# Performance work log

Hardware: AMD Instinct MI355X
Metric: run time of the kernel (lower is better)

## Reference

```python
import jax, jax.numpy as jnp
import numpy as np

B, H, L, D = 16, 8, 512, 64
TEMPERATURE = 8.0  # sqrt(d_k)
MASK_SENTINEL = -10000.0
BIG_NEG = 1e9


def setup_inputs() -> dict:
    key = jax.random.key(0)
    kq, kk, kv, km = jax.random.split(key, 4)
    q = jax.random.normal(kq, (B * H, L, D), dtype=jnp.float32)
    k = jax.random.normal(kk, (B * H, L, D), dtype=jnp.float32)
    v = jax.random.normal(kv, (B * H, L, D), dtype=jnp.float32)
    mask = jnp.where(jax.random.bernoulli(km, 0.1, (B, L)), MASK_SENTINEL, 0.0).astype(jnp.float32)
    return {"q": q, "k": k, "v": v, "mask": mask, "n_head": H}


def reference(q, k, v, mask, n_head):
    # attn: [B*H, L, L]
    attn = jnp.einsum("bid,bjd->bij", q, k) / TEMPERATURE
    # masked_fill(mask == -10000, 1e9); other values subtracted as-is
    m = jnp.where(mask == MASK_SENTINEL, BIG_NEG, mask)          # [B, L]
    m_bh = jnp.repeat(m, n_head, axis=0)                          # [B*H, L], matches reshape(B*H, ...)
    # row mask (mask.unsqueeze(-1).repeat) and its transpose (column mask)
    attn = attn - m_bh[:, :, None] - m_bh[:, None, :]
    attn = jax.nn.softmax(attn, axis=2)
    # dropout in eval mode (identity) for the deterministic reference
    output = jnp.einsum("bij,bjd->bid", attn, v)
    return output, attn
```

## Files before the change

### kernel.cpp

```cpp
#include <hip/hip_runtime.h>
#include <stdint.h>

#define Ln 512
#define Dn 64
#define BHn 128
#define AOFF ((size_t)BHn*Ln*Dn)

typedef __attribute__((ext_vector_type(8))) short short8;
typedef __attribute__((ext_vector_type(4))) float f32x4;
typedef __attribute__((ext_vector_type(4))) unsigned int u32x4;
typedef __attribute__((ext_vector_type(2))) unsigned int u32x2;

__device__ __forceinline__ uint16_t f2bf(float f){
  uint32_t x = __float_as_uint(f);
  return (uint16_t)((x + 0x7FFFu + ((x>>16)&1u)) >> 16);
}
__device__ __forceinline__ float bf2f(uint16_t u){ return __uint_as_float(((uint32_t)u)<<16); }
__device__ __forceinline__ uint32_t pack2(float a, float b){
  return (uint32_t)f2bf(a) | ((uint32_t)f2bf(b)<<16);
}
__device__ __forceinline__ void gld16(const uint16_t* g, uint16_t* l){
  __builtin_amdgcn_global_load_lds(
      (const __attribute__((address_space(1))) void*)g,
      (__attribute__((address_space(3))) void*)l, 16, 0, 0);
}

extern "C" __global__ __launch_bounds__(256)
void attn_prep(const float* __restrict__ kg, const float* __restrict__ vg,
               uint16_t* __restrict__ khw, uint16_t* __restrict__ klw,
               uint16_t* __restrict__ vtw)
{
  const int t  = threadIdx.x;
  const int cx = blockIdx.x;
  const int c  = cx >> 1;
  const int h  = cx & 1;
  const int bh = blockIdx.y;
  const size_t base = (size_t)bh*(Ln*Dn);
  const size_t wsb  = ((size_t)bh<<15) + ((size_t)c<<13);

  {
    const int sj  = h*64 + (t>>2);
    const int skh = (t>>1)&1;
    const int w2b = (t&1)*2;
    const float* kr = kg + base + (size_t)(c*128 + sj)*Dn + skh*32 + w2b*8;
    const int sx = (sj&7)<<3;
    #pragma unroll
    for (int w=0; w<2; ++w){
      const int w2 = w2b + w;
      f32x4 x0 = *(const f32x4*)(kr + w*8);
      f32x4 x1 = *(const f32x4*)(kr + w*8 + 4);
      uint32_t hw[4], lw[4];
      #pragma unroll
      for (int pi=0; pi<4; ++pi){
        float a0 = (pi<2) ? x0[pi*2]   : x1[(pi-2)*2];
        float a1 = (pi<2) ? x0[pi*2+1] : x1[(pi-2)*2+1];
        uint16_t h0 = f2bf(a0), h1 = f2bf(a1);
        hw[pi] = (uint32_t)h0 | ((uint32_t)h1<<16);
        lw[pi] = (uint32_t)f2bf(a0 - bf2f(h0)) | ((uint32_t)f2bf(a1 - bf2f(h1))<<16);
      }
      const size_t di = wsb + sj*64 + ((skh*32 + w2*8) ^ sx);
      *(u32x4*)(khw + di) = (u32x4){hw[0],hw[1],hw[2],hw[3]};
      *(u32x4*)(klw + di) = (u32x4){lw[0],lw[1],lw[2],lw[3]};
    }
  }

  {
    const int j0 = h*64 + (t>>4)*4;
    const int d0 = (t&15)*4;
    const float* vr = vg + base + (size_t)(c*128 + j0)*Dn + d0;
    f32x4 r0 = *(const f32x4*)(vr);
    f32x4 r1 = *(const f32x4*)(vr + Dn);
    f32x4 r2 = *(const f32x4*)(vr + 2*Dn);
    f32x4 r3 = *(const f32x4*)(vr + 3*Dn);
    #pragma unroll
    for (int qd=0; qd<4; ++qd){
      const int d = d0 + qd;
      u32x2 w; w.x = pack2(r0[qd], r1[qd]); w.y = pack2(r2[qd], r3[qd]);
      *(u32x2*)(vtw + wsb + d*128 + (j0 ^ ((d&7)<<3))) = w;
    }
  }
}

extern "C" __global__ __launch_bounds__(256, 2)
void attn_main2(const float* __restrict__ qg, const float* __restrict__ mg,
                const uint16_t* __restrict__ khw, const uint16_t* __restrict__ klw,
                const uint16_t* __restrict__ vtw, float* __restrict__ outg)
{
  __shared__ __align__(16) uint16_t BIG[32768];
  __shared__ float CMV[512];

  const int t    = threadIdx.x;
  const int lane = t & 63;
  const int wv   = t >> 6;
  const int li   = lane & 15;
  const int lq   = lane >> 4;
  const int kx   = (li&7)<<3;

  const int lin = blockIdx.x + (blockIdx.y << 3);
  const int xcd = lin & 7;
  const int jj  = lin >> 3;
  const int bh  = (xcd << 4) + (jj >> 3);
  const int b   = bh >> 3;
  const int i0  = (jj & 7)*64 + wv*16;

  const size_t base = (size_t)bh*(Ln*Dn);
  const float* mrow = mg + b*Ln;
  const size_t wsbh = (size_t)bh << 15;

  uint16_t* PW = BIG + 16384 + wv*2176;

  auto issueK = [&](int c, int bsel){
    const size_t so = wsbh + ((size_t)c<<13) + (wv<<11) + (lane<<3);
    uint16_t* dh = BIG + bsel*16384 + (wv<<11);
    #pragma unroll
    for (int i=0;i<4;++i){
      gld16(khw + so + i*512, dh + i*512);
      gld16(klw + so + i*512, dh + 8192 + i*512);
    }
  };
  auto issueV = [&](int c, int bsel){
    const size_t so = wsbh + ((size_t)c<<13) + (wv<<11) + (lane<<3);
    uint16_t* dv = BIG + bsel*8192 + (wv<<11);
    #pragma unroll
    for (int i=0;i<4;++i) gld16(vtw + so + i*512, dv + i*512);
  };

  const float* qrow = qg + base + (size_t)(i0 + li)*Dn;
  f32x4 qx0a = *(const f32x4*)(qrow + lq*8);
  f32x4 qx0b = *(const f32x4*)(qrow + lq*8 + 4);
  f32x4 qx1a = *(const f32x4*)(qrow + 32 + lq*8);
  f32x4 qx1b = *(const f32x4*)(qrow + 32 + lq*8 + 4);
  float m0 = mrow[t], m1 = mrow[t+256];
  float mv = mrow[i0 + li];

  issueK(0, 0);

  CMV[t]     = (m0 < -9000.f) ? 1e9f : m0;
  CMV[t+256] = (m1 < -9000.f) ? 1e9f : m1;
  const float rmv = (mv < -9000.f) ? 1e9f : mv;

  short8 qhi[2], qlo[2];
  #pragma unroll
  for (int kt=0; kt<2; ++kt){
    f32x4 xa = kt ? qx1a : qx0a;
    f32x4 xb = kt ? qx1b : qx0b;
    #pragma unroll
    for (int e=0; e<8; ++e){
      float x = (e<4) ? xa[e] : xb[e-4];
      uint16_t h = f2bf(x);
      qhi[kt][e] = (short)h;
      qlo[kt][e] = (short)f2bf(x - bf2f(h));
    }
  }

  f32x4 acc[32];
  #pragma unroll
  for (int j=0; j<32; ++j) acc[j] = (f32x4)0.f;

  #pragma unroll
  for (int c=0; c<4; ++c){
    if (c<3) issueK(c+1, (c+1)&1);
    if (c<3) asm volatile("s_waitcnt vmcnt(8)" ::: "memory");
    else     asm volatile("s_waitcnt vmcnt(4)" ::: "memory");
    __builtin_amdgcn_sched_barrier(0);
    __builtin_amdgcn_s_barrier();
    __builtin_amdgcn_sched_barrier(0);
    const uint16_t* KHp = BIG + (c&1)*16384;
    const uint16_t* KLp = KHp + 8192;
    __builtin_amdgcn_s_setprio(1);
    #pragma unroll
    for (int jt=0; jt<8; ++jt){
      #pragma unroll
      for (int kt=0; kt<2; ++kt){
        const int idx = (jt*16 + li)*64 + ((kt*32 + lq*8) ^ kx);
        short8 kh = *(const short8*)(KHp + idx);
        short8 kl = *(const short8*)(KLp + idx);
        f32x4 A = acc[c*8+jt];
        A = __builtin_amdgcn_mfma_f32_16x16x32_bf16(kh, qhi[kt], A, 0,0,0);
        A = __builtin_amdgcn_mfma_f32_16x16x32_bf16(kl, qhi[kt], A, 0,0,0);
        A = __builtin_amdgcn_mfma_f32_16x16x32_bf16(kh, qlo[kt], A, 0,0,0);
        acc[c*8+jt] = A;
      }
    }
    __builtin_amdgcn_s_setprio(0);
    __builtin_amdgcn_sched_barrier(0);
    __builtin_amdgcn_s_barrier();
    __builtin_amdgcn_sched_barrier(0);
    if (c==2) issueV(0, 0);
  }

  #pragma unroll
  for (int jt=0; jt<32; ++jt){
    f32x4 cm = *(const f32x4*)(CMV + jt*16 + lq*4);
    #pragma unroll
    for (int r=0; r<4; ++r)
      acc[jt][r] = (acc[jt][r]*0.125f - rmv) - cm[r];
  }

  float mx = -3.4e38f;
  #pragma unroll
  for (int jt=0; jt<32; ++jt)
    #pragma unroll
    for (int r=0; r<4; ++r) mx = fmaxf(mx, acc[jt][r]);
  mx = fmaxf(mx, __shfl_xor(mx, 16));
  mx = fmaxf(mx, __shfl_xor(mx, 32));
  float sum = 0.f;
  #pragma unroll
  for (int jt=0; jt<32; ++jt)
    #pragma unroll
    for (int r=0; r<4; ++r){ float e = __expf(acc[jt][r]-mx); acc[jt][r] = e; sum += e; }
  sum += __shfl_xor(sum, 16);
  sum += __shfl_xor(sum, 32);
  const float inv = 1.0f/sum;
  #pragma unroll
  for (int jt=0; jt<32; ++jt) acc[jt] = acc[jt]*inv;

  f32x4 oacc[4];
  #pragma unroll
  for (int dt=0; dt<4; ++dt) oacc[dt] = (f32x4)0.f;

  float* arow = outg + AOFF + (size_t)bh*Ln*Ln + (size_t)(i0+li)*Ln;

  #pragma unroll
  for (int c=0; c<4; ++c){
    u32x2 pwreg[8];
    #pragma unroll
    for (int jtl=0; jtl<8; ++jtl){
      const f32x4 p = acc[c*8+jtl];
      pwreg[jtl].x = pack2(p[0], p[1]);
      pwreg[jtl].y = pack2(p[2], p[3]);
    }
    if (c==0) asm volatile("s_waitcnt vmcnt(0)" ::: "memory");
    else      asm volatile("s_waitcnt vmcnt(8)" ::: "memory");
    __builtin_amdgcn_sched_barrier(0);
    __builtin_amdgcn_s_barrier();
    __builtin_amdgcn_sched_barrier(0);
    if (c<3) issueV(c+1, (c+1)&1);
    #pragma unroll
    for (int jtl=0; jtl<8; ++jtl)
      *(u32x2*)(PW + li*136 + jtl*16 + lq*4) = pwreg[jtl];
    asm volatile("s_waitcnt lgkmcnt(0)" ::: "memory");
    __builtin_amdgcn_sched_barrier(0);
    const uint16_t* VTp = BIG + (c&1)*8192;
    __builtin_amdgcn_s_setprio(1);
    #pragma unroll
    for (int c32=0; c32<4; ++c32){
      short8 pf = *(const short8*)(PW + li*136 + c32*32 + lq*8);
      #pragma unroll
      for (int dt=0; dt<4; ++dt){
        short8 vb = *(const short8*)(VTp + (dt*16+li)*128 + ((c32*32+lq*8) ^ kx));
        oacc[dt] = __builtin_amdgcn_mfma_f32_16x16x32_bf16(vb, pf, oacc[dt], 0,0,0);
      }
    }
    __builtin_amdgcn_s_setprio(0);
    #pragma unroll
    for (int jtl=0; jtl<8; ++jtl)
      *(f32x4*)(arow + (c*8+jtl)*16 + lq*4) = acc[c*8+jtl];
  }

  #pragma unroll
  for (int dt=0; dt<4; ++dt)
    *(f32x4*)(outg + base + (size_t)(i0+li)*Dn + dt*16 + lq*4) = oacc[dt];
}

#define KSTR  72
#define VTSTR 136
#define FPSTRH 136

extern "C" __global__ __launch_bounds__(256, 2)
void attn_mfma(const float* __restrict__ qg, const float* __restrict__ kg,
               const float* __restrict__ vg, const float* __restrict__ mg,
               float* __restrict__ outg)
{
  __shared__ uint4 ldsraw[(36864 + 2048)/16];
  uint16_t* KHI = (uint16_t*)ldsraw;
  uint16_t* KLO = KHI + 128*KSTR;
  uint16_t* VT  = (uint16_t*)ldsraw;
  float*    CMV = (float*)((char*)ldsraw + 36864);

  const int t    = threadIdx.x;
  const int lane = t & 63;
  const int wv   = t >> 6;
  const int li   = lane & 15;
  const int lq   = lane >> 4;

  const int lin = blockIdx.x + (blockIdx.y << 3);
  const int xcd = lin & 7;
  const int jj  = lin >> 3;
  const int bh  = (xcd << 4) + (jj >> 3);
  const int b   = bh >> 3;
  const int i0  = (jj & 7)*64 + wv*16;

  const size_t base = (size_t)bh*(Ln*Dn);
  const float* mrow = mg + b*Ln;

  uint16_t* PW = (uint16_t*)((char*)ldsraw + 17408 + wv*(16*FPSTRH*2));

  {
    float m0 = mrow[t], m1 = mrow[t+256];
    CMV[t]     = (m0 < -9000.f) ? 1e9f : m0;
    CMV[t+256] = (m1 < -9000.f) ? 1e9f : m1;
  }

  short8 qhi[2], qlo[2];
  {
    const float* qrow = qg + base + (size_t)(i0 + li)*Dn;
    #pragma unroll
    for (int kt=0; kt<2; ++kt){
      const float* p = qrow + kt*32 + lq*8;
      f32x4 x0 = *(const f32x4*)p;
      f32x4 x1 = *(const f32x4*)(p+4);
      #pragma unroll
      for (int e=0; e<8; ++e){
        float x = (e<4) ? x0[e] : x1[e-4];
        uint16_t h = f2bf(x);
        qhi[kt][e] = (short)h;
        qlo[kt][e] = (short)f2bf(x - bf2f(h));
      }
    }
  }

  f32x4 acc[32];
  #pragma unroll
  for (int j=0; j<32; ++j) acc[j] = (f32x4)0.f;

  const int sj = t>>1, skh = t&1;
  #pragma unroll
  for (int c=0; c<4; ++c){
    __syncthreads();
    {
      const float* kr = kg + base + (size_t)(c*128 + sj)*Dn + skh*32;
      uint16_t* dhi = KHI + sj*KSTR + skh*32;
      uint16_t* dlo = KLO + sj*KSTR + skh*32;
      #pragma unroll
      for (int w2=0; w2<4; ++w2){
        f32x4 x0 = *(const f32x4*)(kr + w2*8);
        f32x4 x1 = *(const f32x4*)(kr + w2*8 + 4);
        uint32_t hw[4], lw[4];
        #pragma unroll
        for (int pi=0; pi<4; ++pi){
          float a0 = (pi<2) ? x0[pi*2]   : x1[(pi-2)*2];
          float a1 = (pi<2) ? x0[pi*2+1] : x1[(pi-2)*2+1];
          uint16_t h0 = f2bf(a0), h1 = f2bf(a1);
          hw[pi] = (uint32_t)h0 | ((uint32_t)h1<<16);
          lw[pi] = (uint32_t)f2bf(a0 - bf2f(h0)) | ((uint32_t)f2bf(a1 - bf2f(h1))<<16);
        }
        *(u32x4*)(dhi + w2*8) = (u32x4){hw[0],hw[1],hw[2],hw[3]};
        *(u32x4*)(dlo + w2*8) = (u32x4){lw[0],lw[1],lw[2],lw[3]};
      }
    }
    __syncthreads();
    #pragma unroll
    for (int jt=0; jt<8; ++jt){
      #pragma unroll
      for (int kt=0; kt<2; ++kt){
        const int off = (jt*16 + li)*KSTR + kt*32 + lq*8;
        short8 kh = *(const short8*)(KHI + off);
        short8 kl = *(const short8*)(KLO + off);
        f32x4 A = acc[c*8+jt];
        A = __builtin_amdgcn_mfma_f32_16x16x32_bf16(kh, qhi[kt], A, 0,0,0);
        A = __builtin_amdgcn_mfma_f32_16x16x32_bf16(kl, qhi[kt], A, 0,0,0);
        A = __builtin_amdgcn_mfma_f32_16x16x32_bf16(kh, qlo[kt], A, 0,0,0);
        acc[c*8+jt] = A;
      }
    }
  }

  {
    float mv = mrow[i0 + li];
    const float rmv = (mv < -9000.f) ? 1e9f : mv;
    #pragma unroll
    for (int jt=0; jt<32; ++jt){
      f32x4 cm = *(const f32x4*)(CMV + jt*16 + lq*4);
      #pragma unroll
      for (int r=0; r<4; ++r)
        acc[jt][r] = (acc[jt][r]*0.125f - rmv) - cm[r];
    }
  }
  float mx = -3.4e38f;
  #pragma unroll
  for (int jt=0; jt<32; ++jt)
    #pragma unroll
    for (int r=0; r<4; ++r) mx = fmaxf(mx, acc[jt][r]);
  mx = fmaxf(mx, __shfl_xor(mx, 16));
  mx = fmaxf(mx, __shfl_xor(mx, 32));
  float sum = 0.f;
  #pragma unroll
  for (int jt=0; jt<32; ++jt)
    #pragma unroll
    for (int r=0; r<4; ++r){ float e = __expf(acc[jt][r]-mx); acc[jt][r] = e; sum += e; }
  sum += __shfl_xor(sum, 16);
  sum += __shfl_xor(sum, 32);
  const float inv = 1.0f/sum;

  {
    float* arow = outg + AOFF + (size_t)bh*Ln*Ln + (size_t)(i0+li)*Ln;
    #pragma unroll
    for (int jt=0; jt<32; ++jt){
      f32x4 p = acc[jt]*inv;
      acc[jt] = p;
      *(f32x4*)(arow + jt*16 + lq*4) = p;
    }
  }

  f32x4 oacc[4];
  #pragma unroll
  for (int dt=0; dt<4; ++dt) oacc[dt] = (f32x4)0.f;

  #pragma unroll
  for (int c=0; c<4; ++c){
    __syncthreads();
    #pragma unroll
    for (int it=0; it<2; ++it){
      const int j0 = (t>>4)*4 + it*64;
      const int d0 = (t&15)*4;
      const float* vr = vg + base + (size_t)(c*128 + j0)*Dn + d0;
      f32x4 r0 = *(const f32x4*)(vr);
      f32x4 r1 = *(const f32x4*)(vr + Dn);
      f32x4 r2 = *(const f32x4*)(vr + 2*Dn);
      f32x4 r3 = *(const f32x4*)(vr + 3*Dn);
      #pragma unroll
      for (int qd=0; qd<4; ++qd){
        u32x2 w; w.x = pack2(r0[qd], r1[qd]); w.y = pack2(r2[qd], r3[qd]);
        *(u32x2*)(VT + (d0+qd)*VTSTR + j0) = w;
      }
    }
    __syncthreads();
    #pragma unroll
    for (int jtl=0; jtl<8; ++jtl){
      const f32x4 p = acc[c*8+jtl];
      u32x2 w; w.x = pack2(p[0], p[1]); w.y = pack2(p[2], p[3]);
      *(u32x2*)(PW + li*FPSTRH + jtl*16 + lq*4) = w;
    }
    asm volatile("s_waitcnt lgkmcnt(0)" ::: "memory");
    #pragma unroll
    for (int c32=0; c32<4; ++c32){
      short8 pf = *(const short8*)(PW + li*FPSTRH + c32*32 + lq*8);
      #pragma unroll
      for (int dt=0; dt<4; ++dt){
        short8 vb = *(const short8*)(VT + (dt*16+li)*VTSTR + c32*32 + lq*8);
        oacc[dt] = __builtin_amdgcn_mfma_f32_16x16x32_bf16(vb, pf, oacc[dt], 0,0,0);
      }
    }
  }

  #pragma unroll
  for (int dt=0; dt<4; ++dt)
    *(f32x4*)(outg + base + (size_t)(i0+li)*Dn + dt*16 + lq*4) = oacc[dt];
}

extern "C" void kernel_launch(void* const* d_in, const int* in_sizes, int n_in,
                              void* d_out, int out_size, void* d_ws, size_t ws_size,
                              hipStream_t stream)
{
  (void)in_sizes; (void)n_in; (void)out_size;
  const float* qg = (const float*)d_in[0];
  const float* kg = (const float*)d_in[1];
  const float* vg = (const float*)d_in[2];
  const float* mg = (const float*)d_in[3];
  float* outg = (float*)d_out;

  const size_t WS_NEED = 25165824;
  if (d_ws && ws_size >= WS_NEED){
    uint16_t* khw = (uint16_t*)d_ws;
    uint16_t* klw = (uint16_t*)((char*)d_ws + 8388608);
    uint16_t* vtw = (uint16_t*)((char*)d_ws + 16777216);
    attn_prep<<<dim3(8, BHn), 256, 0, stream>>>(kg, vg, khw, klw, vtw);
    attn_main2<<<dim3(Ln/64, BHn), 256, 0, stream>>>(qg, mg, khw, klw, vtw, outg);
  } else {
    attn_mfma<<<dim3(Ln/64, BHn), 256, 0, stream>>>(qg, kg, vg, mg, outg);
  }
}
```

Baseline: 216.2 us.

## Split key dimension across wave pairs with 32-row blocks and triple-buffered K/V

```diff
diff --git a/kernel.cpp b/kernel.cpp
--- a/kernel.cpp
+++ b/kernel.cpp
@@ -30,20 +30,21 @@
                uint16_t* __restrict__ khw, uint16_t* __restrict__ klw,
                uint16_t* __restrict__ vtw)
 {
-  const int t  = threadIdx.x;
-  const int cx = blockIdx.x;
-  const int c  = cx >> 1;
-  const int h  = cx & 1;
-  const int bh = blockIdx.y;
+  const int t   = threadIdx.x;
+  const int lin = blockIdx.x + (blockIdx.y << 3);
+  const int xcd = lin & 7;
+  const int by2 = lin >> 3;
+  const int bh  = (xcd << 4) + (by2 >> 3);
+  const int hc  = by2 & 7;
   const size_t base = (size_t)bh*(Ln*Dn);
-  const size_t wsb  = ((size_t)bh<<15) + ((size_t)c<<13);
-
-  {
-    const int sj  = h*64 + (t>>2);
-    const int skh = (t>>1)&1;
-    const int w2b = (t&1)*2;
-    const float* kr = kg + base + (size_t)(c*128 + sj)*Dn + skh*32 + w2b*8;
-    const int sx = (sj&7)<<3;
+  const size_t wsbh = (size_t)bh << 15;
+
+  {
+    const int grow = hc*64 + (t>>2);
+    const int skh  = (t>>1)&1;
+    const int w2b  = (t&1)*2;
+    const float* kr = kg + base + (size_t)grow*Dn + skh*32 + w2b*8;
+    const int sx = (grow&7)<<3;
     #pragma unroll
     for (int w=0; w<2; ++w){
       const int w2 = w2b + w;
@@ -58,16 +59,16 @@
         hw[pi] = (uint32_t)h0 | ((uint32_t)h1<<16);
         lw[pi] = (uint32_t)f2bf(a0 - bf2f(h0)) | ((uint32_t)f2bf(a1 - bf2f(h1))<<16);
       }
-      const size_t di = wsb + sj*64 + ((skh*32 + w2*8) ^ sx);
+      const size_t di = wsbh + (size_t)grow*64 + ((skh*32 + w2*8) ^ sx);
       *(u32x4*)(khw + di) = (u32x4){hw[0],hw[1],hw[2],hw[3]};
       *(u32x4*)(klw + di) = (u32x4){lw[0],lw[1],lw[2],lw[3]};
     }
   }
 
   {
-    const int j0 = h*64 + (t>>4)*4;
+    const int j0 = (t>>4)*4;
     const int d0 = (t&15)*4;
-    const float* vr = vg + base + (size_t)(c*128 + j0)*Dn + d0;
+    const float* vr = vg + base + (size_t)(hc*64 + j0)*Dn + d0;
     f32x4 r0 = *(const f32x4*)(vr);
     f32x4 r1 = *(const f32x4*)(vr + Dn);
     f32x4 r2 = *(const f32x4*)(vr + 2*Dn);
@@ -76,64 +77,68 @@
     for (int qd=0; qd<4; ++qd){
       const int d = d0 + qd;
       u32x2 w; w.x = pack2(r0[qd], r1[qd]); w.y = pack2(r2[qd], r3[qd]);
-      *(u32x2*)(vtw + wsb + d*128 + (j0 ^ ((d&7)<<3))) = w;
-    }
-  }
-}
-
-extern "C" __global__ __launch_bounds__(256, 2)
-void attn_main2(const float* __restrict__ qg, const float* __restrict__ mg,
+      *(u32x2*)(vtw + wsbh + hc*4096 + d*64 + (j0 ^ ((d&7)<<3))) = w;
+    }
+  }
+}
+
+extern "C" __global__ __launch_bounds__(256, 3)
+void attn_main4(const float* __restrict__ qg, const float* __restrict__ mg,
                 const uint16_t* __restrict__ khw, const uint16_t* __restrict__ klw,
                 const uint16_t* __restrict__ vtw, float* __restrict__ outg)
 {
-  __shared__ __align__(16) uint16_t BIG[32768];
+  __shared__ __align__(16) uint16_t BIG[24576];
   __shared__ float CMV[512];
+  __shared__ float MXW[64], SMW[64];
 
   const int t    = threadIdx.x;
   const int lane = t & 63;
   const int wv   = t >> 6;
   const int li   = lane & 15;
   const int lq   = lane >> 4;
+  const int ti   = wv >> 1;
+  const int p    = wv & 1;
   const int kx   = (li&7)<<3;
 
-  const int lin = blockIdx.x + (blockIdx.y << 3);
+  const int lin = blockIdx.x + (blockIdx.y << 4);
   const int xcd = lin & 7;
   const int jj  = lin >> 3;
-  const int bh  = (xcd << 4) + (jj >> 3);
+  const int bh  = (xcd << 4) + (jj >> 4);
   const int b   = bh >> 3;
-  const int i0  = (jj & 7)*64 + wv*16;
+  const int i0  = (jj & 15) * 32;
 
   const size_t base = (size_t)bh*(Ln*Dn);
   const float* mrow = mg + b*Ln;
   const size_t wsbh = (size_t)bh << 15;
 
-  uint16_t* PW = BIG + 16384 + wv*2176;
-
-  auto issueK = [&](int c, int bsel){
-    const size_t so = wsbh + ((size_t)c<<13) + (wv<<11) + (lane<<3);
-    uint16_t* dh = BIG + bsel*16384 + (wv<<11);
-    #pragma unroll
-    for (int i=0;i<4;++i){
+  uint16_t* PW = BIG + 12288 + wv*640;
+
+  auto issueK = [&](int hc, int bs){
+    const size_t so = wsbh + ((size_t)hc<<12) + (wv<<10) + (lane<<3);
+    uint16_t* dh = BIG + bs*8192 + (wv<<10);
+    #pragma unroll
+    for (int i=0;i<2;++i){
       gld16(khw + so + i*512, dh + i*512);
-      gld16(klw + so + i*512, dh + 8192 + i*512);
+      gld16(klw + so + i*512, dh + 4096 + i*512);
     }
   };
-  auto issueV = [&](int c, int bsel){
-    const size_t so = wsbh + ((size_t)c<<13) + (wv<<11) + (lane<<3);
-    uint16_t* dv = BIG + bsel*8192 + (wv<<11);
-    #pragma unroll
-    for (int i=0;i<4;++i) gld16(vtw + so + i*512, dv + i*512);
+  auto issueV = [&](int hc, int bs){
+    const size_t so = wsbh + ((size_t)hc<<12) + (wv<<10) + (lane<<3);
+    uint16_t* dv = BIG + bs*4096 + (wv<<10);
+    #pragma unroll
+    for (int i=0;i<2;++i) gld16(vtw + so + i*512, dv + i*512);
   };
 
-  const float* qrow = qg + base + (size_t)(i0 + li)*Dn;
+  const float* qrow = qg + base + (size_t)(i0 + ti*16 + li)*Dn;
   f32x4 qx0a = *(const f32x4*)(qrow + lq*8);
   f32x4 qx0b = *(const f32x4*)(qrow + lq*8 + 4);
   f32x4 qx1a = *(const f32x4*)(qrow + 32 + lq*8);
   f32x4 qx1b = *(const f32x4*)(qrow + 32 + lq*8 + 4);
   float m0 = mrow[t], m1 = mrow[t+256];
-  float mv = mrow[i0 + li];
+  float mv = mrow[i0 + ti*16 + li];
 
   issueK(0, 0);
+  issueK(1, 1);
 
   CMV[t]     = (m0 < -9000.f) ? 1e9f : m0;
   CMV[t+256] = (m1 < -9000.f) ? 1e9f : m1;
@@ -153,114 +158,135 @@
     }
   }
 
-  f32x4 acc[32];
-  #pragma unroll
-  for (int j=0; j<32; ++j) acc[j] = (f32x4)0.f;
-
-  #pragma unroll
-  for (int c=0; c<4; ++c){
-    if (c<3) issueK(c+1, (c+1)&1);
-    if (c<3) asm volatile("s_waitcnt vmcnt(8)" ::: "memory");
-    else     asm volatile("s_waitcnt vmcnt(4)" ::: "memory");
+  f32x4 acc[16];
+  #pragma unroll
+  for (int m=0; m<16; ++m) acc[m] = (f32x4)0.f;
+
+  #pragma unroll
+  for (int hc=0; hc<8; ++hc){
+    if (hc<7) asm volatile("s_waitcnt vmcnt(4)" ::: "memory");
+    else      asm volatile("s_waitcnt vmcnt(0)" ::: "memory");
     __builtin_amdgcn_sched_barrier(0);
     __builtin_amdgcn_s_barrier();
     __builtin_amdgcn_sched_barrier(0);
-    const uint16_t* KHp = BIG + (c&1)*16384;
-    const uint16_t* KLp = KHp + 8192;
+    if (hc<6) issueK(hc+2, (hc+2)%3);
+    if (hc==7){ issueV(0, 0); issueV(1, 1); }
+    const uint16_t* KHp = BIG + (hc%3)*8192;
+    const uint16_t* KLp = KHp + 4096;
     __builtin_amdgcn_s_setprio(1);
     #pragma unroll
-    for (int jt=0; jt<8; ++jt){
+    for (int u=0; u<2; ++u){
+      const int row = (2*u + p)*16 + li;
       #pragma unroll
       for (int kt=0; kt<2; ++kt){
-        const int idx = (jt*16 + li)*64 + ((kt*32 + lq*8) ^ kx);
+        const int idx = row*64 + ((kt*32 + lq*8) ^ kx);
         short8 kh = *(const short8*)(KHp + idx);
         short8 kl = *(const short8*)(KLp + idx);
-        f32x4 A = acc[c*8+jt];
+        f32x4 A = acc[hc*2+u];
         A = __builtin_amdgcn_mfma_f32_16x16x32_bf16(kh, qhi[kt], A, 0,0,0);
         A = __builtin_amdgcn_mfma_f32_16x16x32_bf16(kl, qhi[kt], A, 0,0,0);
         A = __builtin_amdgcn_mfma_f32_16x16x32_bf16(kh, qlo[kt], A, 0,0,0);
-        acc[c*8+jt] = A;
+        acc[hc*2+u] = A;
       }
     }
     __builtin_amdgcn_s_setprio(0);
+  }
+
+  #pragma unroll
+  for (int m=0; m<16; ++m){
+    const int jt = 4*(m>>1) + 2*(m&1) + p;
+    f32x4 cm = *(const f32x4*)(CMV + jt*16 + lq*4);
+    #pragma unroll
+    for (int r=0; r<4; ++r)
+      acc[m][r] = (acc[m][r]*0.125f - rmv) - cm[r];
+  }
+
+  float mx = -3.4e38f;
+  #pragma unroll
+  for (int m=0; m<16; ++m)
+    #pragma unroll
+    for (int r=0; r<4; ++r) mx = fmaxf(mx, acc[m][r]);
+  mx = fmaxf(mx, __shfl_xor(mx, 16));
+  mx = fmaxf(mx, __shfl_xor(mx, 32));
+  if (lane < 16) MXW[wv*16 + lane] = mx;
+  asm volatile("s_waitcnt lgkmcnt(0)" ::: "memory");
+  __builtin_amdgcn_s_barrier();
+  const float mxa = fmaxf(mx, MXW[(wv^1)*16 + li]);
+
+  float sum = 0.f;
+  #pragma unroll
+  for (int m=0; m<16; ++m)
+    #pragma unroll
+    for (int r=0; r<4; ++r){ float e = __expf(acc[m][r]-mxa); acc[m][r] = e; sum += e; }
+  sum += __shfl_xor(sum, 16);
+  sum += __shfl_xor(sum, 32);
+  if (lane < 16) SMW[wv*16 + lane] = sum;
+  asm volatile("s_waitcnt lgkmcnt(0)" ::: "memory");
+  __builtin_amdgcn_s_barrier();
+  const float inv = 1.0f/(sum + SMW[(wv^1)*16 + li]);
+  #pragma unroll
+  for (int m=0; m<16; ++m) acc[m] = acc[m]*inv;
+
+  f32x4 oacc[4];
+  #pragma unroll
+  for (int dt=0; dt<4; ++dt) oacc[dt] = (f32x4)0.f;
+
+  float* arow = outg + AOFF + (size_t)bh*Ln*Ln + (size_t)(i0 + ti*16 + li)*Ln;
+  const int jb = (2*(lq>>1) + p)*16 + (lq&1)*8;
+
+  #pragma unroll
+  for (int hc=0; hc<8; ++hc){
+    u32x2 pw0, pw1;
+    { const f32x4 a0 = acc[hc*2], a1 = acc[hc*2+1];
+      pw0.x = pack2(a0[0],a0[1]); pw0.y = pack2(a0[2],a0[3]);
+      pw1.x = pack2(a1[0],a1[1]); pw1.y = pack2(a1[2],a1[3]); }
+    if (hc==0)      asm volatile("s_waitcnt vmcnt(2)" ::: "memory");
+    else if (hc<7)  asm volatile("s_waitcnt vmcnt(4)" ::: "memory");
+    else            asm volatile("s_waitcnt vmcnt(2)" ::: "memory");
     __builtin_amdgcn_sched_barrier(0);
     __builtin_amdgcn_s_barrier();
     __builtin_amdgcn_sched_barrier(0);
-    if (c==2) issueV(0, 0);
-  }
-
-  #pragma unroll
-  for (int jt=0; jt<32; ++jt){
-    f32x4 cm = *(const f32x4*)(CMV + jt*16 + lq*4);
-    #pragma unroll
-    for (int r=0; r<4; ++r)
-      acc[jt][r] = (acc[jt][r]*0.125f - rmv) - cm[r];
-  }
-
-  float mx = -3.4e38f;
-  #pragma unroll
-  for (int jt=0; jt<32; ++jt)
-    #pragma unroll
-    for (int r=0; r<4; ++r) mx = fmaxf(mx, acc[jt][r]);
-  mx = fmaxf(mx, __shfl_xor(mx, 16));
-  mx = fmaxf(mx, __shfl_xor(mx, 32));
-  float sum = 0.f;
-  #pragma unroll
-  for (int jt=0; jt<32; ++jt)
-    #pragma unroll
-    for (int r=0; r<4; ++r){ float e = __expf(acc[jt][r]-mx); acc[jt][r] = e; sum += e; }
-  sum += __shfl_xor(sum, 16);
-  sum += __shfl_xor(sum, 32);
-  const float inv = 1.0f/sum;
-  #pragma unroll
-  for (int jt=0; jt<32; ++jt) acc[jt] = acc[jt]*inv;
-
-  f32x4 oacc[4];
-  #pragma unroll
-  for (int dt=0; dt<4; ++dt) oacc[dt] = (f32x4)0.f;
-
-  float* arow = outg + AOFF + (size_t)bh*Ln*Ln + (size_t)(i0+li)*Ln;
-
-  #pragma unroll
-  for (int c=0; c<4; ++c){
-    u32x2 pwreg[8];
-    #pragma unroll
-    for (int jtl=0; jtl<8; ++jtl){
-      const f32x4 p = acc[c*8+jtl];
-      pwreg[jtl].x = pack2(p[0], p[1]);
-      pwreg[jtl].y = pack2(p[2], p[3]);
-    }
-    if (c==0) asm volatile("s_waitcnt vmcnt(0)" ::: "memory");
-    else      asm volatile("s_waitcnt vmcnt(8)" ::: "memory");
-    __builtin_amdgcn_sched_barrier(0);
-    __builtin_amdgcn_s_barrier();
-    __builtin_amdgcn_sched_barrier(0);
-    if (c<3) issueV(c+1, (c+1)&1);
-    #pragma unroll
-    for (int jtl=0; jtl<8; ++jtl)
-      *(u32x2*)(PW + li*136 + jtl*16 + lq*4) = pwreg[jtl];
+    if (hc<6) issueV(hc+2, (hc+2)%3);
+    *(u32x2*)(PW + li*40 + lq*4)      = pw0;
+    *(u32x2*)(PW + li*40 + 16 + lq*4) = pw1;
     asm volatile("s_waitcnt lgkmcnt(0)" ::: "memory");
     __builtin_amdgcn_sched_barrier(0);
-    const uint16_t* VTp = BIG + (c&1)*8192;
+    const uint16_t* VTp = BIG + (hc%3)*4096;
     __builtin_amdgcn_s_setprio(1);
-    #pragma unroll
-    for (int c32=0; c32<4; ++c32){
-      short8 pf = *(const short8*)(PW + li*136 + c32*32 + lq*8);
-      #pragma unroll
-      for (int dt=0; dt<4; ++dt){
-        short8 vb = *(const short8*)(VTp + (dt*16+li)*128 + ((c32*32+lq*8) ^ kx));
-        oacc[dt] = __builtin_amdgcn_mfma_f32_16x16x32_bf16(vb, pf, oacc[dt], 0,0,0);
-      }
+    short8 pf = *(const short8*)(PW + li*40 + lq*8);
+    #pragma unroll
+    for (int dt=0; dt<4; ++dt){
+      short8 vb = *(const short8*)(VTp + (dt*16+li)*64 + (jb ^ kx));
+      oacc[dt] = __builtin_amdgcn_mfma_f32_16x16x32_bf16(vb, pf, oacc[dt], 0,0,0);
     }
     __builtin_amdgcn_s_setprio(0);
-    #pragma unroll
-    for (int jtl=0; jtl<8; ++jtl)
-      *(f32x4*)(arow + (c*8+jtl)*16 + lq*4) = acc[c*8+jtl];
-  }
-
-  #pragma unroll
-  for (int dt=0; dt<4; ++dt)
-    *(f32x4*)(outg + base + (size_t)(i0+li)*Dn + dt*16 + lq*4) = oacc[dt];
+    *(f32x4*)(arow + (4*hc + p)*16 + lq*4)     = acc[hc*2];
+    *(f32x4*)(arow + (4*hc + 2 + p)*16 + lq*4) = acc[hc*2+1];
+  }
+
+  __builtin_amdgcn_sched_barrier(0);
+  __builtin_amdgcn_s_barrier();
+  __builtin_amdgcn_sched_barrier(0);
+  float* ORf = (float*)BIG;
+  if (p == 1){
+    #pragma unroll
+    for (int dt=0; dt<4; ++dt)
+      #pragma unroll
+      for (int r=0; r<4; ++r)
+        ORf[ti*1088 + (dt*16 + lq*4 + r)*17 + li] = oacc[dt][r];
+  }
+  asm volatile("s_waitcnt lgkmcnt(0)" ::: "memory");
+  __builtin_amdgcn_s_barrier();
+  if (p == 0){
+    #pragma unroll
+    for (int dt=0; dt<4; ++dt){
+      f32x4 o;
+      #pragma unroll
+      for (int r=0; r<4; ++r)
+        o[r] = oacc[dt][r] + ORf[ti*1088 + (dt*16 + lq*4 + r)*17 + li];
+      *(f32x4*)(outg + base + (size_t)(i0 + ti*16 + li)*Dn + dt*16 + lq*4) = o;
+    }
+  }
 }
 
 #define KSTR  72
@@ -466,7 +492,7 @@
     uint16_t* klw = (uint16_t*)((char*)d_ws + 8388608);
     uint16_t* vtw = (uint16_t*)((char*)d_ws + 16777216);
     attn_prep<<<dim3(8, BHn), 256, 0, stream>>>(kg, vg, khw, klw, vtw);
-    attn_main2<<<dim3(Ln/64, BHn), 256, 0, stream>>>(qg, mg, khw, klw, vtw, outg);
+    attn_main4<<<dim3(16, BHn), 256, 0, stream>>>(qg, mg, khw, klw, vtw, outg);
   } else {
     attn_mfma<<<dim3(Ln/64, BHn), 256, 0, stream>>>(qg, kg, vg, mg, outg);
   }
```

Result: slower. 222.6 us (+3.0%).
